# Optimization experiments

Hardware: AMD Instinct MI355X
Metric: run time of the kernel (lower is better)

## Reference

```python
import jax, jax.numpy as jnp
import numpy as np

DIM = 1024
NUM_HEADS = 16
HEAD_DIM = DIM // NUM_HEADS
MAX_LEN = 2048
ROPE_BASE = 10000.0


def _rope_tables(n, d, base=ROPE_BASE):
    inv_freq = 1.0 / (base ** (np.arange(0, d, 2, dtype=np.float32) / d))  # [d/2]
    t = np.arange(n, dtype=np.float32)
    freqs = np.outer(t, inv_freq)  # [n, d/2]
    return jnp.asarray(np.cos(freqs)), jnp.asarray(np.sin(freqs))


def _apply_rotary(x, cos, sin):
    # x: [B, H, N, D]; pairs are consecutive elements (2i, 2i+1)
    xe = x[..., 0::2]
    xo = x[..., 1::2]
    # cos/sin: [N, D/2] -> broadcast over B, H
    oe = xe * cos - xo * sin
    oo = xe * sin + xo * cos
    return jnp.stack([oe, oo], axis=-1).reshape(x.shape)


def setup_inputs() -> dict:
    key = jax.random.key(0)
    ks = jax.random.split(key, 11)
    B, T, S = 4, 2048, 2048
    sc = 1.0 / np.sqrt(DIM)
    inp = {
        "query": jax.random.normal(ks[0], (B, T, DIM), jnp.float32),
        "key": jax.random.normal(ks[1], (B, S, DIM), jnp.float32),
        "value": jax.random.normal(ks[2], (B, S, DIM), jnp.float32),
        "Wq": jax.random.normal(ks[3], (DIM, DIM), jnp.float32) * sc,
        "bq": jnp.zeros((DIM,), jnp.float32),
        "Wk": jax.random.normal(ks[4], (DIM, DIM), jnp.float32) * sc,
        "bk": jnp.zeros((DIM,), jnp.float32),
        "Wv": jax.random.normal(ks[5], (DIM, DIM), jnp.float32) * sc,
        "bv": jnp.zeros((DIM,), jnp.float32),
        "Wo": jax.random.normal(ks[6], (DIM, DIM), jnp.float32) * sc,
        "bo": jnp.zeros((DIM,), jnp.float32),
    }
    return inp


def reference(query, key, value, Wq, bq, Wk, bk, Wv, bv, Wo, bo):
    B, T, C = query.shape
    S = key.shape[1]
    H, D = NUM_HEADS, HEAD_DIM
    scale = D ** -0.5

    q = (query @ Wq + bq).reshape(B, T, H, D).transpose(0, 2, 1, 3)  # [B,H,T,D]
    k = (key @ Wk + bk).reshape(B, S, H, D).transpose(0, 2, 1, 3)    # [B,H,S,D]
    v = (value @ Wv + bv).reshape(B, S, H, D).transpose(0, 2, 1, 3)  # [B,H,S,D]

    cos, sin = _rope_tables(max(T, S), D)
    q = _apply_rotary(q, cos[:T], sin[:T])
    k = _apply_rotary(k, cos[:S], sin[:S])

    scores = jnp.einsum("bhtd,bhsd->bhts", q, k) * scale  # [B,H,T,S]
    causal = jnp.tril(jnp.ones((T, S), bool))
    scores = jnp.where(causal[None, None], scores, -jnp.inf)
    att = jax.nn.softmax(scores, axis=-1)

    out = jnp.einsum("bhts,bhsd->bhtd", att, v)  # [B,H,T,D]
    out = out.transpose(0, 2, 1, 3).reshape(B, T, C)
    return out @ Wo + bo
```

## Files before the change

### kernel.cpp

```cpp
#include <hip/hip_runtime.h>
#include <cstdint>
#include <math.h>

typedef __bf16 bf16_t;
typedef __bf16 bf16x8 __attribute__((ext_vector_type(8)));
typedef __bf16 bf16x4 __attribute__((ext_vector_type(4)));
typedef float f32x4 __attribute__((ext_vector_type(4)));

#define MFMA16(a, b, c) __builtin_amdgcn_mfma_f32_16x16x32_bf16((a), (b), (c), 0, 0, 0)

static constexpr int BATCH = 4;
static constexpr int SEQ = 2048;
static constexpr int DIMC = 1024;
static constexpr int NH = 16;
static constexpr int HD = 64;

__device__ __forceinline__ void async_copy16(void* lds, const void* g) {
    __builtin_amdgcn_global_load_lds(
        (const __attribute__((address_space(1))) void*)g,
        (__attribute__((address_space(3))) void*)lds, 16, 0, 0);
}

__device__ __forceinline__ float fast_exp2(float x) {
#if __has_builtin(__builtin_amdgcn_exp2f)
    return __builtin_amdgcn_exp2f(x);
#else
    return __expf(x * 0.6931471805599453f);
#endif
}

__global__ __launch_bounds__(256) void cvt3(const float* __restrict__ q,
                                            const float* __restrict__ k,
                                            const float* __restrict__ v,
                                            bf16_t* __restrict__ out) {
    const float* in = (blockIdx.y == 0) ? q : ((blockIdx.y == 1) ? k : v);
    bf16_t* o = out + (size_t)blockIdx.y * BATCH * SEQ * DIMC;
    const int i = blockIdx.x * 256 + threadIdx.x;
    const float4 f0 = ((const float4*)in)[i * 2];
    const float4 f1 = ((const float4*)in)[i * 2 + 1];
    bf16x8 vv;
    vv[0] = (bf16_t)f0.x; vv[1] = (bf16_t)f0.y; vv[2] = (bf16_t)f0.z; vv[3] = (bf16_t)f0.w;
    vv[4] = (bf16_t)f1.x; vv[5] = (bf16_t)f1.y; vv[6] = (bf16_t)f1.z; vv[7] = (bf16_t)f1.w;
    ((bf16x8*)o)[i] = vv;
}

__global__ __launch_bounds__(256) void transpose_cvt(const float* __restrict__ W0,
                                                     const float* __restrict__ W1,
                                                     const float* __restrict__ W2,
                                                     const float* __restrict__ W3,
                                                     bf16_t* __restrict__ out) {
    const float* Ws[4] = {W0, W1, W2, W3};
    const float* W = Ws[blockIdx.z];
    bf16_t* Wt = out + (size_t)blockIdx.z * DIMC * DIMC;
    __shared__ float tile[32][33];
    const int tx = threadIdx.x & 31;
    const int ty = threadIdx.x >> 5;
    const int x0 = blockIdx.x * 32;
    const int y0 = blockIdx.y * 32;
    #pragma unroll
    for (int j = ty; j < 32; j += 8)
        tile[j][tx] = W[(size_t)(y0 + j) * DIMC + x0 + tx];
    __syncthreads();
    #pragma unroll
    for (int j = ty; j < 32; j += 8)
        Wt[(size_t)(x0 + j) * DIMC + y0 + tx] = (bf16_t)tile[tx][j];
}

__global__ __launch_bounds__(256) void rope_tab(float* __restrict__ cosT, float* __restrict__ sinT) {
    const int idx = blockIdx.x * 256 + threadIdx.x;
    const int t = idx >> 5;
    const int p = idx & 31;
    const float inv = exp2f(-0.41524101186092029f * (float)p);
    const float ang = (float)t * inv;
    float s, c;
    sincosf(ang, &s, &c);
    cosT[idx] = c;
    sinT[idx] = s;
}

#define GEMM_KLOOP(A_, Bt_)                                                             \
    f32x4 acc[4][4] = {};                                                               \
    const int swW = ((lane >> 2) & 3) ^ ((lane >> 4) & 3);         \
    const int rIn = lane >> 2;                                    \
    const int gW = ((lane & 3) ^ swW) * 8;                        \
    const int fR = (l15 & 3) ^ ((l15 >> 2) & 3);                    \
    for (int kt = 0; kt < DIMC / 32; ++kt) {                                            \
        const int k0 = kt * 32;                                                         \
        __syncthreads();                                                                \
        _Pragma("unroll") for (int ci = 0; ci < 2; ++ci) {                              \
            const int c = 2 * w + ci;                                                   \
            async_copy16(&Bs[c * 512], Bt_ + (size_t)(col0 + c * 16 + rIn) * DIMC + k0 + gW); \
            async_copy16(&As[c * 512], A_ + (size_t)(row0 + c * 16 + rIn) * DIMC + k0 + gW);  \
        }                                                                               \
        __syncthreads();                                                                \
        bf16x8 af[4], bfr[4];                                                           \
        _Pragma("unroll") for (int mt = 0; mt < 4; ++mt)                                \
            af[mt] = *(const bf16x8*)&As[(wr * 64 + mt * 16 + l15) * 32 + ((quad ^ fR) << 3)]; \
        _Pragma("unroll") for (int nt = 0; nt < 4; ++nt)                                \
            bfr[nt] = *(const bf16x8*)&Bs[(wc * 64 + nt * 16 + l15) * 32 + ((quad ^ fR) << 3)]; \
        _Pragma("unroll") for (int mt = 0; mt < 4; ++mt)                                \
            _Pragma("unroll") for (int nt = 0; nt < 4; ++nt)                            \
                acc[mt][nt] = MFMA16(af[mt], bfr[nt], acc[mt][nt]);                     \
    }

__global__ __launch_bounds__(256) void gemm_qkv(const bf16_t* __restrict__ Cb,
                                                const bf16_t* __restrict__ Wt3,
                                                const float* __restrict__ bq,
                                                const float* __restrict__ bk,
                                                const float* __restrict__ bv,
                                                bf16_t* __restrict__ Qr,
                                                bf16_t* __restrict__ Kr,
                                                bf16_t* __restrict__ Vr,
                                                const float* __restrict__ cosT,
                                                const float* __restrict__ sinT) {
    __shared__ __align__(16) unsigned char smem[32 * 132 * 4];
    bf16_t* As = (bf16_t*)smem;
    bf16_t* Bs = (bf16_t*)(smem + 8192);
    float* eps = (float*)smem;
    const int z = blockIdx.z;
    const bf16_t* A = Cb + (size_t)z * BATCH * SEQ * DIMC;
    const bf16_t* Bt = Wt3 + (size_t)z * DIMC * DIMC;
    const float* bias = (z == 0) ? bq : ((z == 1) ? bk : bv);
    bf16_t* outp = (z == 0) ? Qr : ((z == 1) ? Kr : Vr);
    const bool rope = (z < 2);
    const int tid = threadIdx.x;
    const int w = tid >> 6;
    const int lane = tid & 63;
    const int l15 = lane & 15;
    const int quad = lane >> 4;
    const int wr = w >> 1, wc = w & 1;
    const int raw = blockIdx.y * 8 + blockIdx.x;
    const int row0 = (raw & 63) * 128, col0 = (raw >> 6) * 128;
    GEMM_KLOOP(A, Bt)
    float bvl[4];
    #pragma unroll
    for (int nt = 0; nt < 4; ++nt) bvl[nt] = bias[col0 + wc * 64 + nt * 16 + l15];
    const int lr = tid >> 3;
    const int cg = tid & 7;
    const int c0 = cg * 16;
    const int h = (col0 + c0) >> 6;
    const int dbase = (col0 + c0) & 63;
    #pragma unroll
    for (int p = 0; p < 4; ++p) {
        __syncthreads();
        #pragma unroll
        for (int nt = 0; nt < 4; ++nt)
            #pragma unroll
            for (int r = 0; r < 4; ++r)
                eps[(wr * 16 + quad * 4 + r) * 132 + wc * 64 + nt * 16 + l15] =
                    acc[p][nt][r] + bvl[nt];
        __syncthreads();
        const int grow = row0 + (lr >> 4) * 64 + p * 16 + (lr & 15);
        const int t = grow & (SEQ - 1);
        const int bb = grow >> 11;
        float vals[16];
        #pragma unroll
        for (int q4 = 0; q4 < 4; ++q4) {
            f32x4 vv = *(const f32x4*)&eps[lr * 132 + c0 + q4 * 4];
            vals[q4 * 4 + 0] = vv[0]; vals[q4 * 4 + 1] = vv[1];
            vals[q4 * 4 + 2] = vv[2]; vals[q4 * 4 + 3] = vv[3];
        }
        bf16x8 o0, o1;
        if (rope) {
            const int pbase = t * 32 + (dbase >> 1);
            const float4 cs0 = *(const float4*)&cosT[pbase];
            const float4 cs1 = *(const float4*)&cosT[pbase + 4];
            const float4 sn0 = *(const float4*)&sinT[pbase];
            const float4 sn1 = *(const float4*)&sinT[pbase + 4];
            const float cc[8] = {cs0.x, cs0.y, cs0.z, cs0.w, cs1.x, cs1.y, cs1.z, cs1.w};
            const float ss[8] = {sn0.x, sn0.y, sn0.z, sn0.w, sn1.x, sn1.y, sn1.z, sn1.w};
            #pragma unroll
            for (int i = 0; i < 8; ++i) {
                const float e = vals[2 * i], o = vals[2 * i + 1];
                const float oe = e * cc[i] - o * ss[i];
                const float oo = e * ss[i] + o * cc[i];
                if (i < 4) { o0[2 * i] = (bf16_t)oe; o0[2 * i + 1] = (bf16_t)oo; }
                else { o1[2 * (i - 4)] = (bf16_t)oe; o1[2 * (i - 4) + 1] = (bf16_t)oo; }
            }
        } else {
            #pragma unroll
            for (int i = 0; i < 8; ++i) o0[i] = (bf16_t)vals[i];
            #pragma unroll
            for (int i = 0; i < 8; ++i) o1[i] = (bf16_t)vals[8 + i];
        }
        bf16_t* dst = outp + (((size_t)bb * NH + h) * SEQ + t) * HD + dbase;
        *(bf16x8*)dst = o0;
        *(bf16x8*)(dst + 8) = o1;
    }
}

__global__ __launch_bounds__(256) void gemm_o(const bf16_t* __restrict__ A,
                                              const bf16_t* __restrict__ Bt,
                                              const float* __restrict__ bias,
                                              float* __restrict__ out) {
    __shared__ __align__(16) unsigned char smem[16384];
    bf16_t* As = (bf16_t*)smem;
    bf16_t* Bs = (bf16_t*)(smem + 8192);
    const int tid = threadIdx.x;
    const int w = tid >> 6;
    const int lane = tid & 63;
    const int l15 = lane & 15;
    const int quad = lane >> 4;
    const int wr = w >> 1, wc = w & 1;
    const int raw = blockIdx.y * 8 + blockIdx.x;
    const int row0 = (raw & 63) * 128, col0 = (raw >> 6) * 128;
    GEMM_KLOOP(A, Bt)
    #pragma unroll
    for (int nt = 0; nt < 4; ++nt) {
        const int col = col0 + wc * 64 + nt * 16 + l15;
        const float bvl = bias[col];
        #pragma unroll
        for (int mt = 0; mt < 4; ++mt) {
            #pragma unroll
            for (int r = 0; r < 4; ++r) {
                const int row = row0 + wr * 64 + mt * 16 + quad * 4 + r;
                out[(size_t)row * DIMC + col] = acc[mt][nt][r] + bvl;
            }
        }
    }
}

__global__ __launch_bounds__(256) void attn_kernel(const bf16_t* __restrict__ Qr,
                                                   const bf16_t* __restrict__ Kr,
                                                   const bf16_t* __restrict__ Vr,
                                                   bf16_t* __restrict__ O) {
    __shared__ bf16_t Ks[64 * 64];
    __shared__ bf16_t Vt[64 * 72];
    __shared__ bf16_t Ps[4][32 * 72];
    const int tid = threadIdx.x;
    const int w = tid >> 6;
    const int lane = tid & 63;
    const int l15 = lane & 15;
    const int quad = lane >> 4;
    const int bh = blockIdx.x;
    const int b = bh >> 4, h = bh & 15;
    const bf16_t* Qb = Qr + (size_t)bh * SEQ * HD;
    const bf16_t* Kb = Kr + (size_t)bh * SEQ * HD;
    const bf16_t* Vb = Vr + (size_t)bh * SEQ * HD;
    const float S2 = 0.18033688011112043f;

    bf16x8 ones;
    #pragma unroll
    for (int j8 = 0; j8 < 8; ++j8) ones[j8] = (bf16_t)1.0f;
    bf16x8 idB[2];
    #pragma unroll
    for (int ch = 0; ch < 2; ++ch)
        #pragma unroll
        for (int j8 = 0; j8 < 8; ++j8)
            idB[ch][j8] = (quad * 8 + j8 == ch * 16 + l15) ? (bf16_t)1.0f : (bf16_t)0.0f;

    const int sIn = lane >> 3;
    const int gK = ((lane & 7) ^ sIn) * 8;
    const int fK = (l15 & 7);

    for (int half = 0; half < 2; ++half) {
        const int j = (half == 0) ? blockIdx.y : 15 - blockIdx.y;
        const int q0 = j * 128;
        bf16x8 qa[2][2];
        #pragma unroll
        for (int mg = 0; mg < 2; ++mg)
            #pragma unroll
            for (int kc = 0; kc < 2; ++kc)
                qa[mg][kc] = *(const bf16x8*)(Qb + (size_t)(q0 + mg * 64 + w * 16 + l15) * HD +
                                              kc * 32 + quad * 8);
        f32x4 acco[2][4] = {};
        f32x4 accl[2] = {};
        const int nIter = 2 * j + 2;
        for (int it = 0; it < nIter; ++it) {
            const int s0 = it * 64;
            __syncthreads();
            #pragma unroll
            for (int ci = 0; ci < 2; ++ci) {
                const int c = 2 * w + ci;
                async_copy16(&Ks[c * 512], Kb + (size_t)(s0 + c * 8 + sIn) * HD + gK);
            }
            {
                const bf16_t* vsrc = Vb + (size_t)(s0 + w * 16 + l15) * HD + quad * 8;
                bf16x8 av0 = *(const bf16x8*)(vsrc);
                bf16x8 av1 = *(const bf16x8*)(vsrc + 32);
                #pragma unroll
                for (int c = 0; c < 4; ++c) {
                    f32x4 zz = {};
                    f32x4 tv = MFMA16((c < 2) ? av0 : av1, idB[c & 1], zz);
                    bf16x4 pk;
                    #pragma unroll
                    for (int r = 0; r < 4; ++r) pk[r] = (bf16_t)tv[r];
                    *(bf16x4*)&Vt[(c * 16 + l15) * 72 + w * 16 + quad * 4] = pk;
                }
            }
            __syncthreads();
            bf16x8 kb[4][2];
            #pragma unroll
            for (int mt = 0; mt < 4; ++mt)
                #pragma unroll
                for (int kc = 0; kc < 2; ++kc)
                    kb[mt][kc] = *(const bf16x8*)&Ks[(mt * 16 + l15) * 64 +
                                                     (((kc * 4 + quad) ^ fK) << 3)];
            #pragma unroll
            for (int mg = 0; mg < 2; ++mg) {
                if (mg == 0 && it == 2 * j + 1) continue;
                const bool diag = (it == 2 * j + mg);
                #pragma unroll
                for (int mt = 0; mt < 4; ++mt) {
                    f32x4 z = {};
                    z = MFMA16(kb[mt][0], qa[mg][0], z);
                    z = MFMA16(kb[mt][1], qa[mg][1], z);
                    bf16x4 pk;
                    #pragma unroll
                    for (int r = 0; r < 4; ++r) {
                        float v = z[r];
                        if (diag && (mt * 16 + quad * 4 + r > w * 16 + l15)) v = -INFINITY;
                        pk[r] = (bf16_t)fast_exp2(S2 * v);
                    }
                    *(bf16x4*)&Ps[w][(mg * 16 + l15) * 72 + mt * 16 + quad * 4] = pk;
                }
            }
            asm volatile("s_waitcnt lgkmcnt(0)" ::: "memory");
            bf16x8 vb[4][2];
            #pragma unroll
            for (int dt = 0; dt < 4; ++dt)
                #pragma unroll
                for (int kc = 0; kc < 2; ++kc)
                    vb[dt][kc] = *(const bf16x8*)&Vt[(dt * 16 + l15) * 72 + kc * 32 + quad * 8];
            #pragma unroll
            for (int mg = 0; mg < 2; ++mg) {
                if (mg == 0 && it == 2 * j + 1) continue;
                const bf16x8 pa0 = *(const bf16x8*)&Ps[w][(mg * 16 + l15) * 72 + quad * 8];
                const bf16x8 pa1 = *(const bf16x8*)&Ps[w][(mg * 16 + l15) * 72 + 32 + quad * 8];
                #pragma unroll
                for (int dt = 0; dt < 4; ++dt) {
                    acco[mg][dt] = MFMA16(pa0, vb[dt][0], acco[mg][dt]);
                    acco[mg][dt] = MFMA16(pa1, vb[dt][1], acco[mg][dt]);
                }
                accl[mg] = MFMA16(pa0, ones, accl[mg]);
                accl[mg] = MFMA16(pa1, ones, accl[mg]);
            }
        }
        #pragma unroll
        for (int mg = 0; mg < 2; ++mg) {
            #pragma unroll
            for (int r = 0; r < 4; ++r) {
                const float inv = 1.0f / accl[mg][r];
                const int trow = q0 + mg * 64 + w * 16 + quad * 4 + r;
                bf16_t* orow = O + ((size_t)(b * SEQ + trow)) * DIMC + h * HD;
                #pragma unroll
                for (int dt = 0; dt < 4; ++dt)
                    orow[dt * 16 + l15] = (bf16_t)(acco[mg][dt][r] * inv);
            }
        }
    }
}

extern "C" void kernel_launch(void* const* d_in, const int* in_sizes, int n_in,
                              void* d_out, int out_size, void* d_ws, size_t ws_size,
                              hipStream_t stream) {
    const float* query = (const float*)d_in[0];
    const float* key = (const float*)d_in[1];
    const float* value = (const float*)d_in[2];
    const float* Wq = (const float*)d_in[3];
    const float* bq = (const float*)d_in[4];
    const float* Wk = (const float*)d_in[5];
    const float* bk = (const float*)d_in[6];
    const float* Wv = (const float*)d_in[7];
    const float* bv = (const float*)d_in[8];
    const float* Wo = (const float*)d_in[9];
    const float* bo = (const float*)d_in[10];

    char* ws = (char*)d_ws;
    const size_t WT_BYTES = (size_t)DIMC * DIMC * sizeof(bf16_t);
    const size_t ACT_BYTES = (size_t)BATCH * SEQ * DIMC * sizeof(bf16_t);
    bf16_t* WT = (bf16_t*)ws;
    bf16_t* WoT = WT + 3 * (size_t)DIMC * DIMC;
    float* cosT = (float*)(ws + 4 * WT_BYTES);
    float* sinT = (float*)(ws + 4 * WT_BYTES + 262144);
    bf16_t* Cb = (bf16_t*)(ws + 4 * WT_BYTES + 2 * 262144);
    bf16_t* Qr = (bf16_t*)((char*)Cb + 3 * ACT_BYTES);
    bf16_t* Kr = (bf16_t*)((char*)Cb + 4 * ACT_BYTES);
    bf16_t* Vr = (bf16_t*)((char*)Cb + 5 * ACT_BYTES);
    bf16_t* Ob = Cb;

    transpose_cvt<<<dim3(32, 32, 4), 256, 0, stream>>>(Wq, Wk, Wv, Wo, WT);
    rope_tab<<<dim3(256), 256, 0, stream>>>(cosT, sinT);
    cvt3<<<dim3(4096, 3), 256, 0, stream>>>(query, key, value, Cb);
    gemm_qkv<<<dim3(DIMC / 128, (BATCH * SEQ) / 128, 3), 256, 0, stream>>>(
        Cb, WT, bq, bk, bv, Qr, Kr, Vr, cosT, sinT);
    attn_kernel<<<dim3(BATCH * NH, 8), 256, 0, stream>>>(Qr, Kr, Vr, Ob);
    gemm_o<<<dim3(DIMC / 128, (BATCH * SEQ) / 128), 256, 0, stream>>>(Ob, WoT, bo, (float*)d_out);
}
```

Before: 340.4 us.

## Double-buffer K/V tiles in attention, fold softmax scale into Q, split grid

The attention kernel now double-buffers the K and V shared-memory tiles. The next tile's async K copy and V global loads are issued before computing on the current tile, which removes one barrier per iteration. The softmax scale (times log2 e) is folded into Q during the QKV GEMM's rope epilogue, so the per-element multiply before exp2 goes away. The grid is doubled to 16 y-blocks, each handling one query block with heaviest blocks scheduled first, instead of pairing blocks for balance. s_setprio hints are added around the MFMA sections. The costs are more LDS use, possible load imbalance from unpaired blocks, and the scale now being applied before the bf16 rounding of Q.

```diff
diff --git a/kernel.cpp b/kernel.cpp
--- a/kernel.cpp
+++ b/kernel.cpp
@@ -162,6 +162,7 @@
         }
         bf16x8 o0, o1;
         if (rope) {
+            const float osc = (z == 0) ? 0.18033688011112043f : 1.0f;
             const int pbase = t * 32 + (dbase >> 1);
             const float4 cs0 = *(const float4*)&cosT[pbase];
             const float4 cs1 = *(const float4*)&cosT[pbase + 4];
@@ -172,8 +173,8 @@
             #pragma unroll
             for (int i = 0; i < 8; ++i) {
                 const float e = vals[2 * i], o = vals[2 * i + 1];
-                const float oe = e * cc[i] - o * ss[i];
-                const float oo = e * ss[i] + o * cc[i];
+                const float oe = (e * cc[i] - o * ss[i]) * osc;
+                const float oo = (e * ss[i] + o * cc[i]) * osc;
                 if (i < 4) { o0[2 * i] = (bf16_t)oe; o0[2 * i + 1] = (bf16_t)oo; }
                 else { o1[2 * (i - 4)] = (bf16_t)oe; o1[2 * (i - 4) + 1] = (bf16_t)oo; }
             }
@@ -224,8 +225,8 @@
                                                    const bf16_t* __restrict__ Kr,
                                                    const bf16_t* __restrict__ Vr,
                                                    bf16_t* __restrict__ O) {
-    __shared__ bf16_t Ks[64 * 64];
-    __shared__ bf16_t Vt[64 * 72];
+    __shared__ bf16_t Ks[2][64 * 64];
+    __shared__ bf16_t Vt[2][64 * 72];
     __shared__ bf16_t Ps[4][32 * 72];
     const int tid = threadIdx.x;
     const int w = tid >> 6;
@@ -237,7 +238,6 @@
     const bf16_t* Qb = Qr + (size_t)bh * SEQ * HD;
     const bf16_t* Kb = Kr + (size_t)bh * SEQ * HD;
     const bf16_t* Vb = Vr + (size_t)bh * SEQ * HD;
-    const float S2 = 0.18033688011112043f;
 
     bf16x8 ones;
     #pragma unroll
@@ -253,102 +253,137 @@
     const int gK = ((lane & 7) ^ sIn) * 8;
     const int fK = (l15 & 7);
 
-    for (int half = 0; half < 2; ++half) {
-        const int j = (half == 0) ? blockIdx.y : 15 - blockIdx.y;
-        const int q0 = j * 128;
-        bf16x8 qa[2][2];
-        #pragma unroll
-        for (int mg = 0; mg < 2; ++mg)
-            #pragma unroll
-            for (int kc = 0; kc < 2; ++kc)
-                qa[mg][kc] = *(const bf16x8*)(Qb + (size_t)(q0 + mg * 64 + w * 16 + l15) * HD +
-                                              kc * 32 + quad * 8);
-        f32x4 acco[2][4] = {};
-        f32x4 accl[2] = {};
-        const int nIter = 2 * j + 2;
-        for (int it = 0; it < nIter; ++it) {
-            const int s0 = it * 64;
-            __syncthreads();
+#define VTRANS(buf, a0, a1)                                                      \
+    {                                                                            \
+        _Pragma("unroll") for (int c = 0; c < 4; ++c) {                          \
+            f32x4 zt = {};                                                       \
+            f32x4 tv = MFMA16((c < 2) ? (a0) : (a1), idB[c & 1], zt);            \
+            bf16x4 pkt;                                                          \
+            _Pragma("unroll") for (int rr = 0; rr < 4; ++rr)                     \
+                pkt[rr] = (bf16_t)tv[rr];                                        \
+            *(bf16x4*)&Vt[buf][(c * 16 + l15) * 72 + w * 16 + quad * 4] = pkt;   \
+        }                                                                        \
+    }
+
+    const int j = 15 - (int)blockIdx.y;
+    const int q0 = j * 128;
+    bf16x8 qa[2][2];
+    #pragma unroll
+    for (int mg = 0; mg < 2; ++mg)
+        #pragma unroll
+        for (int kc = 0; kc < 2; ++kc)
+            qa[mg][kc] = *(const bf16x8*)(Qb + (size_t)(q0 + mg * 64 + w * 16 + l15) * HD +
+                                          kc * 32 + quad * 8);
+    f32x4 acco[2][4] = {};
+    f32x4 accl[2] = {};
+    const int nIter = 2 * j + 2;
+
+    #pragma unroll
+    for (int ci = 0; ci < 2; ++ci) {
+        const int c = 2 * w + ci;
+        async_copy16(&Ks[0][c * 512], Kb + (size_t)(c * 8 + sIn) * HD + gK);
+    }
+    {
+        const bf16_t* vsrc = Vb + (size_t)(w * 16 + l15) * HD + quad * 8;
+        bf16x8 pv0 = *(const bf16x8*)vsrc;
+        bf16x8 pv1 = *(const bf16x8*)(vsrc + 32);
+        VTRANS(0, pv0, pv1);
+    }
+    __syncthreads();
+
+    int cur = 0;
+    for (int it = 0; it < nIter; ++it) {
+        const int nxt = cur ^ 1;
+        const bool hn = (it + 1 < nIter);
+        bf16x8 av0, av1;
+        if (hn) {
+            const int s1 = (it + 1) * 64;
             #pragma unroll
             for (int ci = 0; ci < 2; ++ci) {
                 const int c = 2 * w + ci;
-                async_copy16(&Ks[c * 512], Kb + (size_t)(s0 + c * 8 + sIn) * HD + gK);
-            }
-            {
-                const bf16_t* vsrc = Vb + (size_t)(s0 + w * 16 + l15) * HD + quad * 8;
-                bf16x8 av0 = *(const bf16x8*)(vsrc);
-                bf16x8 av1 = *(const bf16x8*)(vsrc + 32);
+                async_copy16(&Ks[nxt][c * 512], Kb + (size_t)(s1 + c * 8 + sIn) * HD + gK);
+            }
+            const bf16_t* vsrc = Vb + (size_t)(s1 + w * 16 + l15) * HD + quad * 8;
+            av0 = *(const bf16x8*)vsrc;
+            av1 = *(const bf16x8*)(vsrc + 32);
+        }
+        bf16x8 kb[4][2];
+        #pragma unroll
+        for (int mt = 0; mt < 4; ++mt)
+            #pragma unroll
+            for (int kc = 0; kc < 2; ++kc)
+                kb[mt][kc] = *(const bf16x8*)&Ks[cur][(mt * 16 + l15) * 64 +
+                                                      (((kc * 4 + quad) ^ fK) << 3)];
+        const bool skip0 = (it == 2 * j + 1);
+        f32x4 zz[2][4];
+        __builtin_amdgcn_s_setprio(1);
+        #pragma unroll
+        for (int mg = 0; mg < 2; ++mg) {
+            if (mg == 0 && skip0) continue;
+            #pragma unroll
+            for (int mt = 0; mt < 4; ++mt) {
+                f32x4 z = {};
+                z = MFMA16(kb[mt][0], qa[mg][0], z);
+                z = MFMA16(kb[mt][1], qa[mg][1], z);
+                zz[mg][mt] = z;
+            }
+        }
+        __builtin_amdgcn_s_setprio(0);
+        #pragma unroll
+        for (int mg = 0; mg < 2; ++mg) {
+            if (mg == 0 && skip0) continue;
+            const bool diag = (it == 2 * j + mg);
+            #pragma unroll
+            for (int mt = 0; mt < 4; ++mt) {
+                bf16x4 pk;
                 #pragma unroll
-                for (int c = 0; c < 4; ++c) {
-                    f32x4 zz = {};
-                    f32x4 tv = MFMA16((c < 2) ? av0 : av1, idB[c & 1], zz);
-                    bf16x4 pk;
-                    #pragma unroll
-                    for (int r = 0; r < 4; ++r) pk[r] = (bf16_t)tv[r];
-                    *(bf16x4*)&Vt[(c * 16 + l15) * 72 + w * 16 + quad * 4] = pk;
+                for (int r = 0; r < 4; ++r) {
+                    float v = zz[mg][mt][r];
+                    if (diag && (mt * 16 + quad * 4 + r > w * 16 + l15)) v = -INFINITY;
+                    pk[r] = (bf16_t)fast_exp2(v);
                 }
-            }
-            __syncthreads();
-            bf16x8 kb[4][2];
-            #pragma unroll
-            for (int mt = 0; mt < 4; ++mt)
-                #pragma unroll
-                for (int kc = 0; kc < 2; ++kc)
-                    kb[mt][kc] = *(const bf16x8*)&Ks[(mt * 16 + l15) * 64 +
-                                                     (((kc * 4 + quad) ^ fK) << 3)];
-            #pragma unroll
-            for (int mg = 0; mg < 2; ++mg) {
-                if (mg == 0 && it == 2 * j + 1) continue;
-                const bool diag = (it == 2 * j + mg);
-                #pragma unroll
-                for (int mt = 0; mt < 4; ++mt) {
-                    f32x4 z = {};
-                    z = MFMA16(kb[mt][0], qa[mg][0], z);
-                    z = MFMA16(kb[mt][1], qa[mg][1], z);
-                    bf16x4 pk;
-                    #pragma unroll
-                    for (int r = 0; r < 4; ++r) {
-                        float v = z[r];
-                        if (diag && (mt * 16 + quad * 4 + r > w * 16 + l15)) v = -INFINITY;
-                        pk[r] = (bf16_t)fast_exp2(S2 * v);
-                    }
-                    *(bf16x4*)&Ps[w][(mg * 16 + l15) * 72 + mt * 16 + quad * 4] = pk;
-                }
-            }
-            asm volatile("s_waitcnt lgkmcnt(0)" ::: "memory");
-            bf16x8 vb[4][2];
+                *(bf16x4*)&Ps[w][(mg * 16 + l15) * 72 + mt * 16 + quad * 4] = pk;
+            }
+        }
+        asm volatile("s_waitcnt lgkmcnt(0)" ::: "memory");
+        bf16x8 vb[4][2];
+        #pragma unroll
+        for (int dt = 0; dt < 4; ++dt)
+            #pragma unroll
+            for (int kc = 0; kc < 2; ++kc)
+                vb[dt][kc] = *(const bf16x8*)&Vt[cur][(dt * 16 + l15) * 72 + kc * 32 + quad * 8];
+        #pragma unroll
+        for (int mg = 0; mg < 2; ++mg) {
+            if (mg == 0 && skip0) continue;
+            const bf16x8 pa0 = *(const bf16x8*)&Ps[w][(mg * 16 + l15) * 72 + quad * 8];
+            const bf16x8 pa1 = *(const bf16x8*)&Ps[w][(mg * 16 + l15) * 72 + 32 + quad * 8];
+            __builtin_amdgcn_s_setprio(1);
+            #pragma unroll
+            for (int dt = 0; dt < 4; ++dt) {
+                acco[mg][dt] = MFMA16(pa0, vb[dt][0], acco[mg][dt]);
+                acco[mg][dt] = MFMA16(pa1, vb[dt][1], acco[mg][dt]);
+            }
+            accl[mg] = MFMA16(pa0, ones, accl[mg]);
+            accl[mg] = MFMA16(pa1, ones, accl[mg]);
+            __builtin_amdgcn_s_setprio(0);
+        }
+        if (hn) VTRANS(nxt, av0, av1);
+        __syncthreads();
+        cur = nxt;
+    }
+    #pragma unroll
+    for (int mg = 0; mg < 2; ++mg) {
+        #pragma unroll
+        for (int r = 0; r < 4; ++r) {
+            const float inv = 1.0f / accl[mg][r];
+            const int trow = q0 + mg * 64 + w * 16 + quad * 4 + r;
+            bf16_t* orow = O + ((size_t)(b * SEQ + trow)) * DIMC + h * HD;
             #pragma unroll
             for (int dt = 0; dt < 4; ++dt)
-                #pragma unroll
-                for (int kc = 0; kc < 2; ++kc)
-                    vb[dt][kc] = *(const bf16x8*)&Vt[(dt * 16 + l15) * 72 + kc * 32 + quad * 8];
-            #pragma unroll
-            for (int mg = 0; mg < 2; ++mg) {
-                if (mg == 0 && it == 2 * j + 1) continue;
-                const bf16x8 pa0 = *(const bf16x8*)&Ps[w][(mg * 16 + l15) * 72 + quad * 8];
-                const bf16x8 pa1 = *(const bf16x8*)&Ps[w][(mg * 16 + l15) * 72 + 32 + quad * 8];
-                #pragma unroll
-                for (int dt = 0; dt < 4; ++dt) {
-                    acco[mg][dt] = MFMA16(pa0, vb[dt][0], acco[mg][dt]);
-                    acco[mg][dt] = MFMA16(pa1, vb[dt][1], acco[mg][dt]);
-                }
-                accl[mg] = MFMA16(pa0, ones, accl[mg]);
-                accl[mg] = MFMA16(pa1, ones, accl[mg]);
-            }
-        }
-        #pragma unroll
-        for (int mg = 0; mg < 2; ++mg) {
-            #pragma unroll
-            for (int r = 0; r < 4; ++r) {
-                const float inv = 1.0f / accl[mg][r];
-                const int trow = q0 + mg * 64 + w * 16 + quad * 4 + r;
-                bf16_t* orow = O + ((size_t)(b * SEQ + trow)) * DIMC + h * HD;
-                #pragma unroll
-                for (int dt = 0; dt < 4; ++dt)
-                    orow[dt * 16 + l15] = (bf16_t)(acco[mg][dt][r] * inv);
-            }
-        }
-    }
+                orow[dt * 16 + l15] = (bf16_t)(acco[mg][dt][r] * inv);
+        }
+    }
+#undef VTRANS
 }
 
 extern "C" void kernel_launch(void* const* d_in, const int* in_sizes, int n_in,
@@ -384,6 +419,6 @@
     cvt3<<<dim3(4096, 3), 256, 0, stream>>>(query, key, value, Cb);
     gemm_qkv<<<dim3(DIMC / 128, (BATCH * SEQ) / 128, 3), 256, 0, stream>>>(
         Cb, WT, bq, bk, bv, Qr, Kr, Vr, cosT, sinT);
-    attn_kernel<<<dim3(BATCH * NH, 8), 256, 0, stream>>>(Qr, Kr, Vr, Ob);
+    attn_kernel<<<dim3(BATCH * NH, 16), 256, 0, stream>>>(Qr, Kr, Vr, Ob);
     gemm_o<<<dim3(DIMC / 128, (BATCH * SEQ) / 128), 256, 0, stream>>>(Ob, WoT, bo, (float*)d_out);
 }
```

Result: no change. 334.9 us (-1.6%).
